# Kernel tuning notes

Hardware: AMD Instinct MI355X
Metric: run time of the kernel (lower is better)

The kernel has to match this reference:

```python
import jax, jax.numpy as jnp
import numpy as np

B, S, E, H = 2, 1024, 1024, 16
Dh = E // H


def setup_inputs() -> dict:
    key = jax.random.key(0)
    ks = jax.random.split(key, 32)
    sc = 1.0 / np.sqrt(E)  # xavier-ish scale
    inp = {}
    names_x = ["x_q_a", "x_q_b", "x_kv_a", "x_kv_b"]
    for i, n in enumerate(names_x):
        inp[n] = jax.random.normal(ks[i], (B, S, E), jnp.float32)
    # causal mask, broadcastable to (B, H, S, S); masked where == 0
    inp["mask"] = jnp.tril(jnp.ones((S, S), jnp.int32))[None, None, :, :]
    inp["layer_theta"] = jnp.float32(0.3)
    inp["thetas_head"] = 0.1 * jax.random.normal(ks[4], (H,), jnp.float32)
    i = 5
    for p in ["q", "k", "v", "o"]:
        inp[p + "_wa"] = sc * jax.random.normal(ks[i], (E, E), jnp.float32); i += 1
        inp[p + "_wb"] = sc * jax.random.normal(ks[i], (E, E), jnp.float32); i += 1
        inp[p + "_ba"] = jnp.zeros((E,), jnp.float32)
        inp[p + "_bb"] = jnp.zeros((E,), jnp.float32)
    return inp


def _qc_dense(xa, xb, wa, wb, ba, bb, j2):
    # F.linear: x @ W.T + b ; j2 is a scalar so (Wb*j2) factors out
    out_a = xa @ wa.T + ba + (xb @ wb.T) * j2
    out_b = xa @ wb.T + bb + xb @ wa.T
    return out_a, out_b


def _shape(x):
    # (B,S,E) -> (B,H,S,Dh)
    return x.reshape(B, S, H, Dh).transpose(0, 2, 1, 3)


def _unshape(x):
    return x.transpose(0, 2, 1, 3).reshape(B, S, E)


def _rope(x):
    # standard rotate-half RoPE on last dim, positions over axis -2
    inv_freq = 1.0 / (10000.0 ** (jnp.arange(0, Dh, 2, dtype=jnp.float32) / Dh))
    ang = jnp.arange(S, dtype=jnp.float32)[:, None] * inv_freq[None, :]  # (S, Dh/2)
    cos = jnp.concatenate([jnp.cos(ang), jnp.cos(ang)], axis=-1)  # (S, Dh)
    sin = jnp.concatenate([jnp.sin(ang), jnp.sin(ang)], axis=-1)
    x1, x2 = x[..., : Dh // 2], x[..., Dh // 2:]
    rot = jnp.concatenate([-x2, x1], axis=-1)
    return x * cos + rot * sin


def reference(x_q_a, x_q_b, x_kv_a, x_kv_b, mask, layer_theta, thetas_head,
              q_wa, q_wb, q_ba, q_bb, k_wa, k_wb, k_ba, k_bb,
              v_wa, v_wb, v_ba, v_bb, o_wa, o_wb, o_ba, o_bb):
    j2 = jnp.sin(2.0 * layer_theta) - 1.0
    qa, qb = _qc_dense(x_q_a, x_q_b, q_wa, q_wb, q_ba, q_bb, j2)
    ka, kb = _qc_dense(x_kv_a, x_kv_b, k_wa, k_wb, k_ba, k_bb, j2)
    va, vb = _qc_dense(x_kv_a, x_kv_b, v_wa, v_wb, v_ba, v_bb, j2)
    qa, qb = _rope(_shape(qa)), _rope(_shape(qb))
    ka, kb = _rope(_shape(ka)), _rope(_shape(kb))
    va, vb = _shape(va), _shape(vb)
    j2h = (jnp.sin(2.0 * thetas_head) - 1.0).reshape(1, H, 1, 1)
    # dual QC score matrices (B,H,S,S)
    s_a = jnp.einsum("bhqd,bhkd->bhqk", qa, ka) + jnp.einsum("bhqd,bhkd->bhqk", qb, kb) * j2h
    s_b = jnp.einsum("bhqd,bhkd->bhqk", qa, kb) + jnp.einsum("bhqd,bhkd->bhqk", qb, ka)
    mag = jnp.sqrt(s_a * s_a + s_b * s_b + 1e-8) / np.sqrt(Dh)
    mag = jnp.where(mask == 0, -1e9, mag)
    attn = jax.nn.softmax(mag, axis=-1)
    out_a = _unshape(jnp.einsum("bhqk,bhkd->bhqd", attn, va))
    out_b = _unshape(jnp.einsum("bhqk,bhkd->bhqd", attn, vb))
    return _qc_dense(out_a, out_b, o_wa, o_wb, o_ba, o_bb, j2)
```

## Files before the change

### kernel.cpp

```cpp
#include <hip/hip_runtime.h>
#include <math.h>
#include <stdint.h>

#define BATCH 2
#define SEQ   1024
#define EMB   1024
#define NH    16
#define DH    64
#define BSE   (BATCH*SEQ*EMB)
#define MROWS (BATCH*SEQ)

typedef unsigned short u16;
typedef __attribute__((ext_vector_type(8))) short short8;
typedef __attribute__((ext_vector_type(4))) float f32x4;

__device__ __forceinline__ float bf2f(u16 u) {
    return __uint_as_float(((unsigned int)u) << 16);
}
__device__ __forceinline__ u16 f2bf(float f) {
    unsigned int x = __float_as_uint(f);
    x += 0x7FFFu + ((x >> 16) & 1u);
    return (u16)(x >> 16);
}

__device__ __forceinline__ void async_copy16(const void* g, void* l) {
    __builtin_amdgcn_global_load_lds(
        (const __attribute__((address_space(1))) unsigned int*)g,
        (__attribute__((address_space(3))) unsigned int*)l,
        16, 0, 0);
}


struct PackArgs {
    const float* src[24];
    u16*         dst[24];
    int          scaled[24];
};

__global__ __launch_bounds__(256) void pack_kernel(PackArgs pa, const float* __restrict__ theta)
{
    const int e = blockIdx.y;
    const size_t i = ((size_t)blockIdx.x * 256 + threadIdx.x) * 4;
    const int sc_mode = pa.scaled[e];
    if (sc_mode == 2) {
        float4 z = {0.f, 0.f, 0.f, 0.f};
        *(float4*)((float*)pa.dst[e] + i) = z;
        return;
    }
    float sc = 1.0f;
    if (sc_mode == 1) sc = sinf(2.0f * theta[0]) - 1.0f;
    float4 v = *(const float4*)(pa.src[e] + i);
    ushort4 o;
    o.x = f2bf(v.x * sc); o.y = f2bf(v.y * sc);
    o.z = f2bf(v.z * sc); o.w = f2bf(v.w * sc);
    *(ushort4*)(pa.dst[e] + i) = o;
}

struct GemmArgs {
    const u16*   A1s[8];
    const u16*   A2s[8];
    const u16*   Blo[8];
    const u16*   Bhi[8];
    const float* bias[8];
    void*        dst[8];
    int          mode[8];
};

template<int SPLITK>
__global__ __launch_bounds__(256) void mfma_gemm(GemmArgs ga)
{
    __shared__ u16 sA[128][32];
    __shared__ u16 sB[128][32];

    const int t    = threadIdx.x;
    const int lane = t & 63;
    const int w    = t >> 6;
    const int wx   = w & 1;
    const int wy   = w >> 1;
    const int n0   = blockIdx.y * 128;
    const int m0   = blockIdx.x * 128;
    const int ko   = (SPLITK == 2) ? blockIdx.z : 0;
    const int seg  = n0 >> 10;
    const int nloc = n0 & 1023;

    const int srow = t >> 2;
    const int sb   = (t & 3) * 16;

    f32x4 acc[4][4] = {};

    const char* A1 = (const char*)ga.A1s[seg];
    const char* A2 = (const char*)ga.A2s[seg];
    const char* Bl = (const char*)ga.Blo[seg];
    const char* Bh = (const char*)ga.Bhi[seg];
    if (SPLITK == 2 && ko) { A1 = A2; Bl = Bh; }

    const int frow = lane & 15;
    const int quad = lane >> 4;

    const int NKT = (SPLITK == 2) ? 32 : 64;
    for (int kt = 0; kt < NKT; ++kt) {
        const char* As = (SPLITK == 1 && (kt & 32)) ? A2 : A1;
        const char* Bs = (SPLITK == 1 && (kt & 32)) ? Bh : Bl;
        const size_t kbyte = (size_t)(kt & 31) * 64;

        __syncthreads();
        #pragma unroll
        for (int r = 0; r < 2; ++r) {
            const int row = r*64 + srow;
            const int ldsoff = (r*64 + w*16) * 64;
            async_copy16(As + (size_t)(m0 + row)*2048 + kbyte + sb,
                         (char*)&sA[0][0] + ldsoff);
            async_copy16(Bs + (size_t)(nloc + row)*2048 + kbyte + sb,
                         (char*)&sB[0][0] + ldsoff);
        }
        __syncthreads();

        short8 af[4], bfr[4];
        #pragma unroll
        for (int i = 0; i < 4; ++i)
            af[i] = *(const short8*)&sA[wy*64 + i*16 + frow][quad*8];
        #pragma unroll
        for (int j = 0; j < 4; ++j)
            bfr[j] = *(const short8*)&sB[wx*64 + j*16 + frow][quad*8];

        #pragma unroll
        for (int i = 0; i < 4; ++i)
            #pragma unroll
            for (int j = 0; j < 4; ++j)
                acc[i][j] = __builtin_amdgcn_mfma_f32_16x16x32_bf16(
                                af[i], bfr[j], acc[i][j], 0, 0, 0);
    }

    const float* bias = ga.bias[seg];
    const int mode = ga.mode[seg];

    #pragma unroll
    for (int j = 0; j < 4; ++j) {
        const int c = nloc + wx*64 + j*16 + frow;
        const float bv = (SPLITK == 2 && ko) ? 0.0f : bias[c];
        #pragma unroll
        for (int i = 0; i < 4; ++i) {
            #pragma unroll
            for (int reg = 0; reg < 4; ++reg) {
                const int m = m0 + wy*64 + i*16 + quad*4 + reg;
                const float val = acc[i][j][reg] + bv;
                if (mode == 1) {
                    if (SPLITK == 2)
                        atomicAdd((float*)ga.dst[seg] + (size_t)m*1024 + c, val);
                    else
                        ((float*)ga.dst[seg])[(size_t)m*1024 + c] = val;
                } else if (mode == 2) {
                    ((u16*)ga.dst[seg])[((size_t)(m >> 10) << 20) + (size_t)c*1024 + (m & 1023)] = f2bf(val);
                } else {
                    ((u16*)ga.dst[seg])[(size_t)m*1024 + c] = f2bf(val);
                }
            }
        }
    }
}

__global__ __launch_bounds__(256) void rope_kernel(
    u16* qa, u16* qb, u16* ka, u16* kb)
{
    u16* p;
    switch (blockIdx.y) {
        case 0:  p = qa; break;
        case 1:  p = qb; break;
        case 2:  p = ka; break;
        default: p = kb; break;
    }
    const int i   = blockIdx.x * 256 + threadIdx.x;
    const int d   = i & 31;
    const int hh  = (i >> 5) & (NH - 1);
    const int row = i >> 9;
    const int s   = row & (SEQ - 1);
    const size_t base = (size_t)row * EMB + hh * DH;

    float x1 = bf2f(p[base + d]);
    float x2 = bf2f(p[base + d + 32]);
    const float invf_rev = expf(-(float)d * 0.28782313662425576f) * 0.15915494309189535f;
    float rev = (float)s * invf_rev;
    rev -= floorf(rev);
    const float sn = __builtin_amdgcn_sinf(rev);
    const float cs = __builtin_amdgcn_cosf(rev);
    p[base + d]      = f2bf(x1 * cs - x2 * sn);
    p[base + d + 32] = f2bf(x2 * cs + x1 * sn);
}

__global__ __launch_bounds__(256) void attn_mfma(
    const u16* __restrict__ qa, const u16* __restrict__ qb,
    const u16* __restrict__ ka, const u16* __restrict__ kb,
    const u16* __restrict__ vat, const u16* __restrict__ vbt,
    const float* __restrict__ thetas,
    u16* __restrict__ oa, u16* __restrict__ ob)
{
    __shared__ u16 sKa[64][64];
    __shared__ u16 sKb[64][64];
    __shared__ u16 sVa[64][64];
    __shared__ u16 sVb[64][64];
    __shared__ u16 sP[4][16][72];

    const int t    = threadIdx.x;
    const int lane = t & 63;
    const int w    = t >> 6;
    const int L15  = lane & 15;
    const int quad = lane >> 4;

    const int bid  = blockIdx.x;
    const int aa   = (bid >> 5) & 7;
    const int qt   = (bid >> 8) ? aa : (15 - aa);
    const int bh   = bid & 31;
    const int h    = bh & 15;
    const int b    = bh >> 4;

    const float j2h = sinf(2.0f * thetas[h]) - 1.0f;

    const int   qrow  = qt*64 + w*16 + L15;
    const size_t qbase = (size_t)(b*SEQ + qrow) * EMB + h*DH;
    short8 fqa[2], fqb[2], fjqb[2];
    fqa[0] = *(const short8*)(qa + qbase + quad*8);
    fqa[1] = *(const short8*)(qa + qbase + 32 + quad*8);
    fqb[0] = *(const short8*)(qb + qbase + quad*8);
    fqb[1] = *(const short8*)(qb + qbase + 32 + quad*8);
    #pragma unroll
    for (int s2 = 0; s2 < 2; ++s2) {
        short8 src = fqb[s2], dst;
        #pragma unroll
        for (int j = 0; j < 8; ++j)
            dst[j] = (short)f2bf(bf2f((u16)src[j]) * j2h);
        fjqb[s2] = dst;
    }

    f32x4 acc_a[4] = {};
    f32x4 acc_b[4] = {};
    float l_lane[4] = {0.f, 0.f, 0.f, 0.f};

    const int subrow = lane >> 3;
    const int g      = (lane & 7) ^ subrow;
    const int swz    = L15 & 7;

    for (int kt = 0; kt <= qt; ++kt) {
        __syncthreads();
        #pragma unroll
        for (int i = 0; i < 2; ++i) {
            const int row = w*16 + i*8 + subrow;
            const int ldsoff = (w*16 + i*8) * 128;
            const size_t ktok = (size_t)(b*SEQ + kt*64 + row);
            async_copy16((const char*)ka + ktok*2048 + h*128 + g*16,
                         (char*)&sKa[0][0] + ldsoff);
            async_copy16((const char*)kb + ktok*2048 + h*128 + g*16,
                         (char*)&sKb[0][0] + ldsoff);
            const size_t vrow = (size_t)b*1048576 + (size_t)(h*64 + row)*1024 + kt*64;
            async_copy16((const char*)vat + vrow*2 + g*16,
                         (char*)&sVa[0][0] + ldsoff);
            async_copy16((const char*)vbt + vrow*2 + g*16,
                         (char*)&sVb[0][0] + ldsoff);
        }
        __syncthreads();

        f32x4 sa[4] = {}, sb[4] = {};
        #pragma unroll
        for (int n = 0; n < 4; ++n) {
            const u16* rKa = &sKa[n*16 + L15][0];
            const u16* rKb = &sKb[n*16 + L15][0];
            short8 ka0 = *(const short8*)(rKa + (( quad      ^ swz) << 3));
            short8 ka1 = *(const short8*)(rKa + (((4 + quad) ^ swz) << 3));
            short8 kb0 = *(const short8*)(rKb + (( quad      ^ swz) << 3));
            short8 kb1 = *(const short8*)(rKb + (((4 + quad) ^ swz) << 3));
            sa[n] = __builtin_amdgcn_mfma_f32_16x16x32_bf16(fqa[0],  ka0, sa[n], 0, 0, 0);
            sa[n] = __builtin_amdgcn_mfma_f32_16x16x32_bf16(fqa[1],  ka1, sa[n], 0, 0, 0);
            sa[n] = __builtin_amdgcn_mfma_f32_16x16x32_bf16(fjqb[0], kb0, sa[n], 0, 0, 0);
            sa[n] = __builtin_amdgcn_mfma_f32_16x16x32_bf16(fjqb[1], kb1, sa[n], 0, 0, 0);
            sb[n] = __builtin_amdgcn_mfma_f32_16x16x32_bf16(fqa[0],  kb0, sb[n], 0, 0, 0);
            sb[n] = __builtin_amdgcn_mfma_f32_16x16x32_bf16(fqa[1],  kb1, sb[n], 0, 0, 0);
            sb[n] = __builtin_amdgcn_mfma_f32_16x16x32_bf16(fqb[0],  ka0, sb[n], 0, 0, 0);
            sb[n] = __builtin_amdgcn_mfma_f32_16x16x32_bf16(fqb[1],  ka1, sb[n], 0, 0, 0);
        }

        float p[4][4];
        if (kt == qt) {
            #pragma unroll
            for (int n = 0; n < 4; ++n)
                #pragma unroll
                for (int r = 0; r < 4; ++r) {
                    const float A = sa[n][r], B = sb[n][r];
                    const float mag = __builtin_amdgcn_sqrtf(A*A + B*B + 1e-8f) * 0.125f;
                    const bool masked = (n*16 + L15) > (w*16 + quad*4 + r);
                    p[n][r] = masked ? 0.0f
                                     : __builtin_amdgcn_exp2f(mag * 1.44269504f);
                }
        } else {
            #pragma unroll
            for (int n = 0; n < 4; ++n)
                #pragma unroll
                for (int r = 0; r < 4; ++r) {
                    const float A = sa[n][r], B = sb[n][r];
                    const float mag = __builtin_amdgcn_sqrtf(A*A + B*B + 1e-8f) * 0.125f;
                    p[n][r] = __builtin_amdgcn_exp2f(mag * 1.44269504f);
                }
        }
        #pragma unroll
        for (int r = 0; r < 4; ++r)
            l_lane[r] += (p[0][r] + p[1][r]) + (p[2][r] + p[3][r]);

        #pragma unroll
        for (int n = 0; n < 4; ++n)
            #pragma unroll
            for (int r = 0; r < 4; ++r)
                sP[w][quad*4 + r][n*16 + L15] = f2bf(p[n][r]);

        short8 pf0 = *(const short8*)&sP[w][L15][quad*8];
        short8 pf1 = *(const short8*)&sP[w][L15][32 + quad*8];

        #pragma unroll
        for (int n = 0; n < 4; ++n) {
            const u16* rVa = &sVa[n*16 + L15][0];
            const u16* rVb = &sVb[n*16 + L15][0];
            short8 va0 = *(const short8*)(rVa + (( quad      ^ swz) << 3));
            short8 va1 = *(const short8*)(rVa + (((4 + quad) ^ swz) << 3));
            short8 vb0 = *(const short8*)(rVb + (( quad      ^ swz) << 3));
            short8 vb1 = *(const short8*)(rVb + (((4 + quad) ^ swz) << 3));
            acc_a[n] = __builtin_amdgcn_mfma_f32_16x16x32_bf16(pf0, va0, acc_a[n], 0, 0, 0);
            acc_a[n] = __builtin_amdgcn_mfma_f32_16x16x32_bf16(pf1, va1, acc_a[n], 0, 0, 0);
            acc_b[n] = __builtin_amdgcn_mfma_f32_16x16x32_bf16(pf0, vb0, acc_b[n], 0, 0, 0);
            acc_b[n] = __builtin_amdgcn_mfma_f32_16x16x32_bf16(pf1, vb1, acc_b[n], 0, 0, 0);
        }
    }

    float inv[4];
    #pragma unroll
    for (int r = 0; r < 4; ++r) {
        float l = l_lane[r];
        #pragma unroll
        for (int off = 8; off >= 1; off >>= 1)
            l += __shfl_xor(l, off, 64);
        inv[r] = 1.0f / l;
    }

    #pragma unroll
    for (int reg = 0; reg < 4; ++reg) {
        const size_t tok = (size_t)(b*SEQ + qt*64 + w*16 + quad*4 + reg);
        #pragma unroll
        for (int n = 0; n < 4; ++n) {
            const size_t idx = tok*EMB + h*DH + n*16 + L15;
            oa[idx] = f2bf(acc_a[n][reg] * inv[reg]);
            ob[idx] = f2bf(acc_b[n][reg] * inv[reg]);
        }
    }
}

extern "C" void kernel_launch(void* const* d_in, const int* in_sizes, int n_in,
                              void* d_out, int out_size, void* d_ws, size_t ws_size,
                              hipStream_t stream)
{
    const float* x_q_a  = (const float*)d_in[0];
    const float* x_q_b  = (const float*)d_in[1];
    const float* x_kv_a = (const float*)d_in[2];
    const float* x_kv_b = (const float*)d_in[3];
    const float* theta    = (const float*)d_in[5];
    const float* thetas_h = (const float*)d_in[6];
    const float* q_wa = (const float*)d_in[7];
    const float* q_wb = (const float*)d_in[8];
    const float* q_ba = (const float*)d_in[9];
    const float* q_bb = (const float*)d_in[10];
    const float* k_wa = (const float*)d_in[11];
    const float* k_wb = (const float*)d_in[12];
    const float* k_ba = (const float*)d_in[13];
    const float* k_bb = (const float*)d_in[14];
    const float* v_wa = (const float*)d_in[15];
    const float* v_wb = (const float*)d_in[16];
    const float* v_ba = (const float*)d_in[17];
    const float* v_bb = (const float*)d_in[18];
    const float* o_wa = (const float*)d_in[19];
    const float* o_wb = (const float*)d_in[20];
    const float* o_ba = (const float*)d_in[21];
    const float* o_bb = (const float*)d_in[22];

    u16* W = (u16*)d_ws;
    const size_t XN = (size_t)BSE;
    const size_t WN = (size_t)EMB*EMB;
    u16* xq_a16  = W;
    u16* xq_b16  = W + XN;
    u16* xkv_a16 = W + 2*XN;
    u16* xkv_b16 = W + 3*XN;
    u16* wbase   = W + 4*XN;
    u16* q_wa16  = wbase;
    u16* q_wb16  = wbase + WN;
    u16* k_wa16  = wbase + 2*WN;
    u16* k_wb16  = wbase + 3*WN;
    u16* v_wa16  = wbase + 4*WN;
    u16* v_wb16  = wbase + 5*WN;
    u16* o_wa16  = wbase + 6*WN;
    u16* o_wb16  = wbase + 7*WN;
    u16* q_wbs16 = wbase + 8*WN;
    u16* k_wbs16 = wbase + 9*WN;
    u16* v_wbs16 = wbase + 10*WN;
    u16* o_wbs16 = wbase + 11*WN;
    u16* qkv     = wbase + 12*WN;
    u16* qa16 = qkv;
    u16* qb16 = qkv + XN;
    u16* ka16 = qkv + 2*XN;
    u16* kb16 = qkv + 3*XN;
    u16* vat16 = qkv + 4*XN;
    u16* vbt16 = qkv + 5*XN;
    u16* ao16 = xq_a16;
    u16* bo16 = xq_b16;

    float* out_a = (float*)d_out;
    float* out_b = out_a + (size_t)BSE;

    PackArgs pa;
    int si = 0;
    auto add = [&](const float* s, u16* d, int scaled, int chunks) {
        for (int c = 0; c < chunks; ++c) {
            pa.src[si] = s ? (s + (size_t)c * WN) : nullptr;
            pa.dst[si] = d + (size_t)c * WN * (scaled == 2 ? 2 : 1);
            pa.scaled[si] = scaled;
            ++si;
        }
    };
    add(x_q_a,  xq_a16,  0, 2);
    add(x_q_b,  xq_b16,  0, 2);
    add(x_kv_a, xkv_a16, 0, 2);
    add(x_kv_b, xkv_b16, 0, 2);
    add(q_wa, q_wa16, 0, 1);  add(q_wb, q_wb16, 0, 1);
    add(k_wa, k_wa16, 0, 1);  add(k_wb, k_wb16, 0, 1);
    add(v_wa, v_wa16, 0, 1);  add(v_wb, v_wb16, 0, 1);
    add(o_wa, o_wa16, 0, 1);  add(o_wb, o_wb16, 0, 1);
    add(q_wb, q_wbs16, 1, 1); add(k_wb, k_wbs16, 1, 1);
    add(v_wb, v_wbs16, 1, 1); add(o_wb, o_wbs16, 1, 1);
    add(nullptr, (u16*)d_out, 2, 4);
    pack_kernel<<<dim3(WN/1024, 24), 256, 0, stream>>>(pa, theta);

    GemmArgs g12;
    const u16* a1s[6] = { xq_a16, xq_a16, xkv_a16, xkv_a16, xkv_a16, xkv_a16 };
    const u16* a2s[6] = { xq_b16, xq_b16, xkv_b16, xkv_b16, xkv_b16, xkv_b16 };
    const u16* blo[6] = { q_wa16, q_wb16, k_wa16, k_wb16, v_wa16, v_wb16 };
    const u16* bhi[6] = { q_wbs16, q_wa16, k_wbs16, k_wa16, v_wbs16, v_wa16 };
    const float* bia[6] = { q_ba, q_bb, k_ba, k_bb, v_ba, v_bb };
    void* dsts[6] = { qa16, qb16, ka16, kb16, vat16, vbt16 };
    const int modes[6] = { 0, 0, 0, 0, 2, 2 };
    for (int s = 0; s < 6; ++s) {
        g12.A1s[s] = a1s[s]; g12.A2s[s] = a2s[s];
        g12.Blo[s] = blo[s]; g12.Bhi[s] = bhi[s];
        g12.bias[s] = bia[s]; g12.dst[s] = dsts[s]; g12.mode[s] = modes[s];
    }
    for (int s = 6; s < 8; ++s) {
        g12.A1s[s] = a1s[0]; g12.A2s[s] = a2s[0];
        g12.Blo[s] = blo[0]; g12.Bhi[s] = bhi[0];
        g12.bias[s] = bia[0]; g12.dst[s] = dsts[0]; g12.mode[s] = 0;
    }
    mfma_gemm<1><<<dim3(MROWS/128, 48), 256, 0, stream>>>(g12);

    rope_kernel<<<dim3((BATCH*SEQ*NH*32)/256, 4), 256, 0, stream>>>(qa16, qb16, ka16, kb16);

    attn_mfma<<<BATCH*NH*(SEQ/64), 256, 0, stream>>>(qa16, qb16, ka16, kb16,
                                                     vat16, vbt16, thetas_h, ao16, bo16);

    GemmArgs g3;
    for (int s = 0; s < 8; ++s) {
        g3.A1s[s] = ao16; g3.A2s[s] = bo16;
        g3.Blo[s] = o_wa16; g3.Bhi[s] = o_wbs16;
        g3.bias[s] = o_ba; g3.dst[s] = out_a; g3.mode[s] = 1;
    }
    g3.Blo[1] = o_wb16; g3.Bhi[1] = o_wa16; g3.bias[1] = o_bb; g3.dst[1] = out_b;
    mfma_gemm<2><<<dim3(MROWS/128, 16, 2), 256, 0, stream>>>(g3);
}
```

Before: 304.2 us.

## Split-K the QKV projection GEMM into bf16 partials reduced in RoPE/V finish kernels

The QKV projection GEMM now runs with a split-K factor of two, doubling the grid, which was 16x48 blocks. Each K-half writes bf16 partial results to a separate workspace region. New rope_finish and v_finish kernels sum the two partials, add bias and apply RoPE or copy V. The goal is more parallelism and better CU occupancy on the first GEMM, paid for with extra partial-buffer traffic, one more kernel launch, and an extra bf16 rounding of each partial. A fallback keeps the old path when the workspace is too small.

```diff
diff --git a/kernel.cpp b/kernel.cpp
--- a/kernel.cpp
+++ b/kernel.cpp
@@ -9,6 +9,7 @@
 #define DH    64
 #define BSE   (BATCH*SEQ*EMB)
 #define MROWS (BATCH*SEQ)
+#define PART  ((size_t)2097152)
 
 typedef unsigned short u16;
 typedef __attribute__((ext_vector_type(8))) short short8;
@@ -29,7 +30,6 @@
         (__attribute__((address_space(3))) unsigned int*)l,
         16, 0, 0);
 }
-
 
 struct PackArgs {
     const float* src[24];
@@ -137,7 +137,7 @@
     #pragma unroll
     for (int j = 0; j < 4; ++j) {
         const int c = nloc + wx*64 + j*16 + frow;
-        const float bv = (SPLITK == 2 && ko) ? 0.0f : bias[c];
+        const float bv = (SPLITK == 2 && (ko || mode != 1)) ? 0.0f : bias[c];
         #pragma unroll
         for (int i = 0; i < 4; ++i) {
             #pragma unroll
@@ -150,9 +150,11 @@
                     else
                         ((float*)ga.dst[seg])[(size_t)m*1024 + c] = val;
                 } else if (mode == 2) {
-                    ((u16*)ga.dst[seg])[((size_t)(m >> 10) << 20) + (size_t)c*1024 + (m & 1023)] = f2bf(val);
+                    u16* d16 = (u16*)ga.dst[seg] + (SPLITK == 2 ? (size_t)ko*PART : 0);
+                    d16[((size_t)(m >> 10) << 20) + (size_t)c*1024 + (m & 1023)] = f2bf(val);
                 } else {
-                    ((u16*)ga.dst[seg])[(size_t)m*1024 + c] = f2bf(val);
+                    u16* d16 = (u16*)ga.dst[seg] + (SPLITK == 2 ? (size_t)ko*PART : 0);
+                    d16[(size_t)m*1024 + c] = f2bf(val);
                 }
             }
         }
@@ -185,6 +187,59 @@
     const float cs = __builtin_amdgcn_cosf(rev);
     p[base + d]      = f2bf(x1 * cs - x2 * sn);
     p[base + d + 32] = f2bf(x2 * cs + x1 * sn);
+}
+
+__global__ __launch_bounds__(256) void rope_finish(
+    const u16* __restrict__ qa_p, const u16* __restrict__ qb_p,
+    const u16* __restrict__ ka_p, const u16* __restrict__ kb_p,
+    const float* __restrict__ q_ba, const float* __restrict__ q_bb,
+    const float* __restrict__ k_ba, const float* __restrict__ k_bb,
+    u16* qa, u16* qb, u16* ka, u16* kb)
+{
+    const u16* p; const float* bias; u16* o;
+    switch (blockIdx.y) {
+        case 0:  p = qa_p; bias = q_ba; o = qa; break;
+        case 1:  p = qb_p; bias = q_bb; o = qb; break;
+        case 2:  p = ka_p; bias = k_ba; o = ka; break;
+        default: p = kb_p; bias = k_bb; o = kb; break;
+    }
+    const int i   = blockIdx.x * 256 + threadIdx.x;
+    const int d   = i & 31;
+    const int hh  = (i >> 5) & (NH - 1);
+    const int row = i >> 9;
+    const int s   = row & (SEQ - 1);
+    const size_t base = (size_t)row * EMB + hh * DH;
+    const int c1  = hh * DH + d;
+
+    float x1 = bf2f(p[base + d])      + bf2f(p[PART + base + d])      + bias[c1];
+    float x2 = bf2f(p[base + d + 32]) + bf2f(p[PART + base + d + 32]) + bias[c1 + 32];
+    const float invf_rev = expf(-(float)d * 0.28782313662425576f) * 0.15915494309189535f;
+    float rev = (float)s * invf_rev;
+    rev -= floorf(rev);
+    const float sn = __builtin_amdgcn_sinf(rev);
+    const float cs = __builtin_amdgcn_cosf(rev);
+    o[base + d]      = f2bf(x1 * cs - x2 * sn);
+    o[base + d + 32] = f2bf(x2 * cs + x1 * sn);
+}
+
+__global__ __launch_bounds__(256) void v_finish(
+    const u16* __restrict__ va_p, const u16* __restrict__ vb_p,
+    const float* __restrict__ v_ba, const float* __restrict__ v_bb,
+    u16* __restrict__ vat, u16* __restrict__ vbt)
+{
+    const u16* p  = blockIdx.y ? vb_p : va_p;
+    const float* bias = blockIdx.y ? v_bb : v_ba;
+    u16* dst = blockIdx.y ? vbt : vat;
+    const size_t i = ((size_t)blockIdx.x * 256 + threadIdx.x) * 4;
+    ushort4 a = *(const ushort4*)(p + i);
+    ushort4 b = *(const ushort4*)(p + PART + i);
+    const float bv = bias[(int)((i >> 10) & 1023)];
+    ushort4 o;
+    o.x = f2bf(bf2f(a.x) + bf2f(b.x) + bv);
+    o.y = f2bf(bf2f(a.y) + bf2f(b.y) + bv);
+    o.z = f2bf(bf2f(a.z) + bf2f(b.z) + bv);
+    o.w = f2bf(bf2f(a.w) + bf2f(b.w) + bv);
+    *(ushort4*)(dst + i) = o;
 }
 
 __global__ __launch_bounds__(256) void attn_mfma(
@@ -406,6 +461,13 @@
     u16* ao16 = xq_a16;
     u16* bo16 = xq_b16;
 
+    u16* partq = qkv + 6*XN;
+    u16* qa_p = partq;            u16* qb_p = partq + 2*PART;
+    u16* ka_p = partq + 4*PART;   u16* kb_p = partq + 6*PART;
+    u16* va_p = partq + 8*PART;   u16* vb_p = partq + 10*PART;
+    const size_t needed = (size_t)((char*)(partq + 12*PART) - (char*)d_ws);
+    const bool use_split = (ws_size >= needed);
+
     float* out_a = (float*)d_out;
     float* out_b = out_a + (size_t)BSE;
 
@@ -438,21 +500,40 @@
     const u16* blo[6] = { q_wa16, q_wb16, k_wa16, k_wb16, v_wa16, v_wb16 };
     const u16* bhi[6] = { q_wbs16, q_wa16, k_wbs16, k_wa16, v_wbs16, v_wa16 };
     const float* bia[6] = { q_ba, q_bb, k_ba, k_bb, v_ba, v_bb };
-    void* dsts[6] = { qa16, qb16, ka16, kb16, vat16, vbt16 };
     const int modes[6] = { 0, 0, 0, 0, 2, 2 };
-    for (int s = 0; s < 6; ++s) {
-        g12.A1s[s] = a1s[s]; g12.A2s[s] = a2s[s];
-        g12.Blo[s] = blo[s]; g12.Bhi[s] = bhi[s];
-        g12.bias[s] = bia[s]; g12.dst[s] = dsts[s]; g12.mode[s] = modes[s];
-    }
-    for (int s = 6; s < 8; ++s) {
-        g12.A1s[s] = a1s[0]; g12.A2s[s] = a2s[0];
-        g12.Blo[s] = blo[0]; g12.Bhi[s] = bhi[0];
-        g12.bias[s] = bia[0]; g12.dst[s] = dsts[0]; g12.mode[s] = 0;
-    }
-    mfma_gemm<1><<<dim3(MROWS/128, 48), 256, 0, stream>>>(g12);
-
-    rope_kernel<<<dim3((BATCH*SEQ*NH*32)/256, 4), 256, 0, stream>>>(qa16, qb16, ka16, kb16);
+    if (use_split) {
+        void* dsts[6] = { qa_p, qb_p, ka_p, kb_p, va_p, vb_p };
+        for (int s = 0; s < 6; ++s) {
+            g12.A1s[s] = a1s[s]; g12.A2s[s] = a2s[s];
+            g12.Blo[s] = blo[s]; g12.Bhi[s] = bhi[s];
+            g12.bias[s] = bia[s]; g12.dst[s] = dsts[s]; g12.mode[s] = modes[s];
+        }
+        for (int s = 6; s < 8; ++s) {
+            g12.A1s[s] = a1s[0]; g12.A2s[s] = a2s[0];
+            g12.Blo[s] = blo[0]; g12.Bhi[s] = bhi[0];
+            g12.bias[s] = bia[0]; g12.dst[s] = dsts[0]; g12.mode[s] = 0;
+        }
+        mfma_gemm<2><<<dim3(MROWS/128, 48, 2), 256, 0, stream>>>(g12);
+        rope_finish<<<dim3((BATCH*SEQ*NH*32)/256, 4), 256, 0, stream>>>(
+            qa_p, qb_p, ka_p, kb_p, q_ba, q_bb, k_ba, k_bb,
+            qa16, qb16, ka16, kb16);
+        v_finish<<<dim3(BSE/1024, 2), 256, 0, stream>>>(
+            va_p, vb_p, v_ba, v_bb, vat16, vbt16);
+    } else {
+        void* dsts[6] = { qa16, qb16, ka16, kb16, vat16, vbt16 };
+        for (int s = 0; s < 6; ++s) {
+            g12.A1s[s] = a1s[s]; g12.A2s[s] = a2s[s];
+            g12.Blo[s] = blo[s]; g12.Bhi[s] = bhi[s];
+            g12.bias[s] = bia[s]; g12.dst[s] = dsts[s]; g12.mode[s] = modes[s];
+        }
+        for (int s = 6; s < 8; ++s) {
+            g12.A1s[s] = a1s[0]; g12.A2s[s] = a2s[0];
+            g12.Blo[s] = blo[0]; g12.Bhi[s] = bhi[0];
+            g12.bias[s] = bia[0]; g12.dst[s] = dsts[0]; g12.mode[s] = 0;
+        }
+        mfma_gemm<1><<<dim3(MROWS/128, 48), 256, 0, stream>>>(g12);
+        rope_kernel<<<dim3((BATCH*SEQ*NH*32)/256, 4), 256, 0, stream>>>(qa16, qb16, ka16, kb16);
+    }
 
     attn_mfma<<<BATCH*NH*(SEQ/64), 256, 0, stream>>>(qa16, qb16, ka16, kb16,
                                                      vat16, vbt16, thetas_h, ao16, bo16);
```

Measured after the change: 322.0 us. 5.9% more time.
